# Kernel optimization log

Measured on AMD Instinct MI355X. Metric: run time of the kernel, lower is better.

Reference implementation:

```python
import jax, jax.numpy as jnp
import numpy as np

# Mamba2 derived dims (headdim=64, ngroups=1, mamba_ssm defaults)
D_MODEL = 1024
D_STATE = 64
D_CONV = 4
EXPAND = 2
D_INNER = EXPAND * D_MODEL          # 2048
HEADDIM = 64
NHEADS = D_INNER // HEADDIM          # 32
CONV_DIM = D_INNER + 2 * D_STATE     # 2176 (x, B, C share the depthwise conv)
D_IN_PROJ = 2 * D_INNER + 2 * D_STATE + NHEADS  # 4256 (z, xBC, dt)
BATCH, SEQ = 8, 1024


def setup_inputs() -> dict:
    key = jax.random.key(0)
    ks = jax.random.split(key, 8)
    g = lambda k, shp, sc=0.02: (jax.random.normal(k, shp, jnp.float32) * sc)
    # dt_bias init as in mamba_ssm: inverse-softplus of dt ~ U[1e-3, 1e-1] (log-uniform)
    dt = jnp.exp(jax.random.uniform(ks[3], (NHEADS,), jnp.float32)
                 * (jnp.log(0.1) - jnp.log(0.001)) + jnp.log(0.001))
    dt_bias = dt + jnp.log(-jnp.expm1(-dt))  # softplus^{-1}(dt)
    A_log = jnp.log(jax.random.uniform(ks[4], (NHEADS,), jnp.float32, 1.0, 16.0))
    return {
        "x": jax.random.normal(ks[0], (BATCH, SEQ, D_MODEL), jnp.float32),
        "W_in": g(ks[1], (D_MODEL, D_IN_PROJ)),
        "conv_w": g(ks[2], (D_CONV, CONV_DIM), 0.2),
        "conv_b": jnp.zeros((CONV_DIM,), jnp.float32),
        "dt_bias": dt_bias,
        "A_log": A_log,
        "Dskip": jnp.ones((NHEADS,), jnp.float32),
        "norm_w": jnp.ones((D_INNER,), jnp.float32),
        "W_out": g(ks[5], (D_INNER, D_MODEL)),
        "head_w": g(ks[6], (D_MODEL, 1)),
        "head_b": jnp.zeros((1,), jnp.float32),
    }


def _mamba2(x, W_in, conv_w, conv_b, dt_bias, A_log, Dskip, norm_w, W_out):
    b, l, _ = x.shape
    zxbcdt = x @ W_in                                   # (b, l, 4256)
    z = zxbcdt[..., :D_INNER]
    xBC = zxbcdt[..., D_INNER:D_INNER + CONV_DIM]
    dt = jax.nn.softplus(zxbcdt[..., D_INNER + CONV_DIM:] + dt_bias)  # (b, l, h)
    # causal depthwise conv1d (kernel D_CONV) + SiLU
    pad = jnp.pad(xBC, ((0, 0), (D_CONV - 1, 0), (0, 0)))
    conv = conv_b + sum(pad[:, k:k + l, :] * conv_w[k] for k in range(D_CONV))
    xBC = jax.nn.silu(conv)
    xh = xBC[..., :D_INNER].reshape(b, l, NHEADS, HEADDIM)
    B = xBC[..., D_INNER:D_INNER + D_STATE]             # (b, l, s) ngroups=1
    C = xBC[..., D_INNER + D_STATE:]                    # (b, l, s)
    A = -jnp.exp(A_log)                                 # (h,)
    dA = jnp.exp(dt * A)                                # (b, l, h)

    def step(h, inps):
        dA_t, dt_t, B_t, C_t, x_t = inps                # (b,h),(b,h),(b,s),(b,s),(b,h,p)
        h = h * dA_t[:, :, None, None] + (dt_t[:, :, None] * x_t)[..., None] * B_t[:, None, None, :]
        y = jnp.einsum('bhps,bs->bhp', h, C_t)
        return h, y

    tm = lambda a: jnp.moveaxis(a, 1, 0)                # time-major for scan
    h0 = jnp.zeros((b, NHEADS, HEADDIM, D_STATE), x.dtype)
    _, y = jax.lax.scan(step, h0, (tm(dA), tm(dt), tm(B), tm(C), tm(xh)))
    y = jnp.moveaxis(y, 0, 1) + Dskip[None, None, :, None] * xh   # skip connection
    # gated RMSNorm: norm(y * silu(z)) * weight
    y = y.reshape(b, l, D_INNER) * jax.nn.silu(z)
    y = y * jax.lax.rsqrt(jnp.mean(y * y, axis=-1, keepdims=True) + 1e-5) * norm_w
    return y @ W_out                                    # (b, l, d_model)


def reference(x, W_in, conv_w, conv_b, dt_bias, A_log, Dskip, norm_w, W_out, head_w, head_b):
    y = _mamba2(x, W_in, conv_w, conv_b, dt_bias, A_log, Dskip, norm_w, W_out)
    return y @ head_w + head_b                          # (b, l, 1)
```

## Files before the change

kernel.cpp:

```cpp
#include <hip/hip_runtime.h>
#include <hip/hip_bf16.h>

#define D_MODEL   1024
#define D_STATE   64
#define D_INNER   2048
#define NHEADS    32
#define CONV_DIM  2176
#define D_IN_PROJ 4256
#define NPAD      4352
#define BATCH     8
#define SEQ       1024
#define NROWS     8192
#define NCHUNK    8
#define CLEN      128

typedef __attribute__((ext_vector_type(8))) short bf16x8;
typedef __attribute__((ext_vector_type(4))) float f32x4;

__device__ __forceinline__ float bf2f(unsigned short u){
  unsigned v = ((unsigned)u) << 16;
  return __builtin_bit_cast(float, v);
}
__device__ __forceinline__ unsigned short f2bf(float f){
  __hip_bfloat16 h = __float2bfloat16(f);
  return __builtin_bit_cast(unsigned short, h);
}

__global__ __launch_bounds__(256) void k_prep(const float* __restrict__ x,
                                              const float* __restrict__ W_in,
                                              const float* __restrict__ W_out,
                                              const float* __restrict__ head_w,
                                              const float* __restrict__ norm_w,
                                              unsigned short* __restrict__ xb,
                                              unsigned short* __restrict__ wt,
                                              float* __restrict__ nwc){
  int blk = blockIdx.x;
  if (blk < 8192){
    int i = blk*256 + threadIdx.x;
    float4 v = ((const float4*)x)[i];
    ushort4 o;
    o.x = f2bf(v.x); o.y = f2bf(v.y); o.z = f2bf(v.z); o.w = f2bf(v.w);
    ((ushort4*)xb)[i] = o;
  } else if (blk < 12544){
    __shared__ float tile[32][33];
    int bx = blk - 8192;
    int n0 = (bx % 136) * 32;
    int k0 = (bx / 136) * 32;
    int tx = threadIdx.x & 31;
    int ty = threadIdx.x >> 5;
    #pragma unroll
    for (int i = 0; i < 4; ++i){
      int kk = ty + i*8;
      int n  = n0 + tx;
      tile[kk][tx] = (n < D_IN_PROJ) ? W_in[(size_t)(k0+kk)*D_IN_PROJ + n] : 0.f;
    }
    __syncthreads();
    #pragma unroll
    for (int i = 0; i < 4; ++i){
      int nn = ty + i*8;
      wt[(size_t)(n0+nn)*D_MODEL + k0 + tx] = f2bf(tile[tx][nn]);
    }
  } else {
    int d    = (blk - 12544)*4 + (threadIdx.x >> 6);
    int lane = threadIdx.x & 63;
    const float* row = W_out + (size_t)d * D_MODEL;
    float s = 0.f;
    #pragma unroll
    for (int k = lane; k < D_MODEL; k += 64) s += row[k] * head_w[k];
    #pragma unroll
    for (int off = 32; off; off >>= 1) s += __shfl_down(s, off);
    if (lane == 0) nwc[d] = s * norm_w[d];
  }
}

__global__ __launch_bounds__(512, 1) void k_gemm256(const unsigned short* __restrict__ A,
                                                    const unsigned short* __restrict__ BT,
                                                    unsigned short* __restrict__ C){
  __shared__ unsigned short smem[65536];
  int bid  = blockIdx.x;
  int lt   = (bid & 7) * 68 + (bid >> 3);
  int m0   = (lt / 17) << 8;
  int n0   = (lt % 17) << 8;
  int tid  = threadIdx.x;
  int w    = tid >> 6, lane = tid & 63;
  int wr   = w >> 2, wc = w & 3;
  int stR  = tid >> 3;
  int stCs = (((tid & 7) ^ ((tid >> 3) & 7)) << 3);
  int wb   = w << 9;
  int frow = lane & 15, fk = (lane >> 4) << 3;

  f32x4 acc[8][4];
  #pragma unroll
  for (int i = 0; i < 8; ++i)
    #pragma unroll
    for (int j = 0; j < 4; ++j) acc[i][j] = (f32x4){0.f,0.f,0.f,0.f};

  const unsigned short* sA0 = A  + (size_t)(m0 + stR)*D_MODEL + stCs;
  const unsigned short* sB0 = BT + (size_t)(n0 + stR)*D_MODEL + stCs;

#define GLD(dstOff, src) __builtin_amdgcn_global_load_lds( \
    (const __attribute__((address_space(1))) void*)(src), \
    (__attribute__((address_space(3))) void*)(smem + (dstOff) + wb), 16, 0, 0)
#define ISSA(bb,kt,i) GLD((bb)*32768 + (i)*4096, \
    sA0 + (size_t)(kt)*64 + (size_t)(i)*64*D_MODEL)
#define ISSB(bb,kt,i) GLD((bb)*32768 + 16384 + (i)*4096, \
    sB0 + (size_t)(kt)*64 + (size_t)(i)*64*D_MODEL)
#define RD8(base, r, col) (*(const bf16x8*)((base) + (r)*64 + ((col) ^ (((r)&7)<<3))))

  ISSB(0,0,0); ISSB(0,0,1); ISSB(0,0,2); ISSB(0,0,3);
  ISSA(0,0,0); ISSA(0,0,2); ISSA(0,0,1); ISSA(0,0,3);
  asm volatile("s_waitcnt vmcnt(2)" ::: "memory");
  __builtin_amdgcn_s_barrier();
  asm volatile("" ::: "memory");

  for (int t = 0; t < 16; ++t){
    int cur = t & 1, nxt = cur ^ 1;
    bool iss = (t < 15);
    const unsigned short* At = smem + cur*32768;
    const unsigned short* Bt = At + 16384;

    bf16x8 bF[4][2];
    if (iss){ ISSB(nxt, t+1, 0); ISSB(nxt, t+1, 1); }
    #pragma unroll
    for (int nf = 0; nf < 4; ++nf){
      int r = wc*64 + nf*16 + frow;
      bF[nf][0] = RD8(Bt, r, fk);
      bF[nf][1] = RD8(Bt, r, 32 + fk);
    }
    {
      bf16x8 aF[2][2];
      #pragma unroll
      for (int mi = 0; mi < 2; ++mi){
        int r = wr*128 + mi*16 + frow;
        aF[mi][0] = RD8(At, r, fk);
        aF[mi][1] = RD8(At, r, 32 + fk);
      }
      __builtin_amdgcn_s_setprio(1);
      #pragma unroll
      for (int mi = 0; mi < 2; ++mi)
        #pragma unroll
        for (int nf = 0; nf < 4; ++nf)
          #pragma unroll
          for (int kki = 0; kki < 2; ++kki)
            acc[mi][nf] = __builtin_amdgcn_mfma_f32_16x16x32_bf16(aF[mi][kki], bF[nf][kki], acc[mi][nf], 0, 0, 0);
      __builtin_amdgcn_s_setprio(0);
    }
    if (iss){ ISSB(nxt, t+1, 2); ISSB(nxt, t+1, 3); }
    {
      bf16x8 aF[2][2];
      #pragma unroll
      for (int mi = 0; mi < 2; ++mi){
        int r = wr*128 + (2 + mi)*16 + frow;
        aF[mi][0] = RD8(At, r, fk);
        aF[mi][1] = RD8(At, r, 32 + fk);
      }
      __builtin_amdgcn_s_setprio(1);
      #pragma unroll
      for (int mi = 0; mi < 2; ++mi)
        #pragma unroll
        for (int nf = 0; nf < 4; ++nf)
          #pragma unroll
          for (int kki = 0; kki < 2; ++kki)
            acc[2 + mi][nf] = __builtin_amdgcn_mfma_f32_16x16x32_bf16(aF[mi][kki], bF[nf][kki], acc[2 + mi][nf], 0, 0, 0);
      __builtin_amdgcn_s_setprio(0);
    }
    if (iss) asm volatile("s_waitcnt vmcnt(4)" ::: "memory");
    else     asm volatile("s_waitcnt vmcnt(0)" ::: "memory");
    __builtin_amdgcn_s_barrier();
    asm volatile("" ::: "memory");
    if (iss){ ISSA(nxt, t+1, 0); ISSA(nxt, t+1, 2); }
    {
      bf16x8 aF[2][2];
      #pragma unroll
      for (int mi = 0; mi < 2; ++mi){
        int r = wr*128 + (4 + mi)*16 + frow;
        aF[mi][0] = RD8(At, r, fk);
        aF[mi][1] = RD8(At, r, 32 + fk);
      }
      __builtin_amdgcn_s_setprio(1);
      #pragma unroll
      for (int mi = 0; mi < 2; ++mi)
        #pragma unroll
        for (int nf = 0; nf < 4; ++nf)
          #pragma unroll
          for (int kki = 0; kki < 2; ++kki)
            acc[4 + mi][nf] = __builtin_amdgcn_mfma_f32_16x16x32_bf16(aF[mi][kki], bF[nf][kki], acc[4 + mi][nf], 0, 0, 0);
      __builtin_amdgcn_s_setprio(0);
    }
    if (iss){ ISSA(nxt, t+1, 1); ISSA(nxt, t+1, 3); }
    {
      bf16x8 aF[2][2];
      #pragma unroll
      for (int mi = 0; mi < 2; ++mi){
        int r = wr*128 + (6 + mi)*16 + frow;
        aF[mi][0] = RD8(At, r, fk);
        aF[mi][1] = RD8(At, r, 32 + fk);
      }
      __builtin_amdgcn_s_setprio(1);
      #pragma unroll
      for (int mi = 0; mi < 2; ++mi)
        #pragma unroll
        for (int nf = 0; nf < 4; ++nf)
          #pragma unroll
          for (int kki = 0; kki < 2; ++kki)
            acc[6 + mi][nf] = __builtin_amdgcn_mfma_f32_16x16x32_bf16(aF[mi][kki], bF[nf][kki], acc[6 + mi][nf], 0, 0, 0);
      __builtin_amdgcn_s_setprio(0);
    }
    if (iss) asm volatile("s_waitcnt vmcnt(2)" ::: "memory");
    else     asm volatile("s_waitcnt vmcnt(0)" ::: "memory");
    __builtin_amdgcn_s_barrier();
    asm volatile("" ::: "memory");
  }
#undef GLD
#undef ISSA
#undef ISSB
#undef RD8

  int crow = (lane >> 4) << 2, ccol = lane & 15;
  #pragma unroll
  for (int mf = 0; mf < 8; ++mf)
    #pragma unroll
    for (int nf = 0; nf < 4; ++nf){
      size_t base = (size_t)(m0 + wr*128 + mf*16 + crow)*NPAD + (n0 + wc*64 + nf*16 + ccol);
      #pragma unroll
      for (int r = 0; r < 4; ++r)
        C[base + (size_t)r*NPAD] = f2bf(acc[mf][nf][r]);
    }
}

__global__ __launch_bounds__(64) void k_dtcs(const unsigned short* __restrict__ zx,
                                             const float* __restrict__ dt_bias,
                                             const float* __restrict__ A_log,
                                             float* __restrict__ dtb,
                                             float* __restrict__ csb,
                                             float* __restrict__ cumA){
  int id = blockIdx.x;
  int bh = id >> 3, c = id & 7;
  int b  = bh >> 5, h = bh & 31;
  int l  = threadIdx.x;
  int t0 = c << 7;
  size_t r0 = (size_t)(b*SEQ + t0 + 2*l);
  float bias = dt_bias[h];
  float raw0 = bf2f(zx[r0*NPAD + D_INNER + CONV_DIM + h]) + bias;
  float raw1 = bf2f(zx[(r0+1)*NPAD + D_INNER + CONV_DIM + h]) + bias;
  float d0 = (raw0 > 20.f) ? raw0 : log1pf(expf(raw0));
  float d1 = (raw1 > 20.f) ? raw1 : log1pf(expf(raw1));
  dtb[(size_t)bh*1024 + t0 + 2*l]     = d0;
  dtb[(size_t)bh*1024 + t0 + 2*l + 1] = d1;
  float pr = d0 + d1;
  float s  = pr;
  #pragma unroll
  for (int off = 1; off < 64; off <<= 1){
    float n = __shfl_up(s, off);
    if (l >= off) s += n;
  }
  float excl = s - pr;
  csb[(size_t)id*128 + 2*l]     = excl + d0;
  csb[(size_t)id*128 + 2*l + 1] = excl + pr;
  if (l == 63){
    float A = -expf(A_log[h]);
    cumA[id] = expf(A * s);
  }
}

__global__ __launch_bounds__(256) void k_conv(const unsigned short* __restrict__ zx,
                                              const float* __restrict__ conv_w,
                                              const float* __restrict__ conv_b,
                                              unsigned short* __restrict__ xbc,
                                              unsigned short* __restrict__ bc16){
  int r = blockIdx.x;
  int l = r & (SEQ - 1);
  for (int oc = threadIdx.x; oc < 272; oc += 256){
    int c = oc * 8;
    float acc[8];
    #pragma unroll
    for (int j = 0; j < 8; ++j) acc[j] = conv_b[c + j];
    #pragma unroll
    for (int k = 0; k < 4; ++k){
      int dl = l + k - 3;
      if (dl >= 0){
        bf16x8 v = *(const bf16x8*)(zx + (size_t)(r + k - 3)*NPAD + D_INNER + c);
        #pragma unroll
        for (int j = 0; j < 8; ++j)
          acc[j] = fmaf(bf2f((unsigned short)v[j]), conv_w[k*CONV_DIM + c + j], acc[j]);
      }
    }
    bf16x8 o;
    #pragma unroll
    for (int j = 0; j < 8; ++j){
      float s = acc[j] / (1.f + expf(-acc[j]));
      o[j] = (short)f2bf(s);
    }
    if (c < D_INNER) *(bf16x8*)(xbc  + (size_t)r*D_INNER + c) = o;
    else             *(bf16x8*)(bc16 + (size_t)r*128 + (c - D_INNER)) = o;
  }
}

__global__ __launch_bounds__(256) void k_ssd1(const unsigned short* __restrict__ xbc,
                                              const unsigned short* __restrict__ bc16,
                                              const float* __restrict__ dtb,
                                              const float* __restrict__ csb,
                                              const float* __restrict__ A_log,
                                              unsigned short* __restrict__ hend){
  __shared__ __align__(16) unsigned short XTw[64*136];
  __shared__ __align__(16) unsigned short BTl[64*136];
  int id = blockIdx.x;
  int bh = id >> 3, c = id & 7;
  int b  = bh >> 5, h = bh & 31;
  int tid = threadIdx.x;
  int w = tid >> 6, l = tid & 63;
  float A = -expf(A_log[h]);
  int row0 = b*SEQ + (c << 7);
  float csT = csb[(size_t)id*128 + 127];

  #pragma unroll
  for (int it = 0; it < 4; ++it){
    int idx = it*256 + tid;
    int tau = idx >> 3, pb = idx & 7;
    bf16x8 v = *(const bf16x8*)(xbc + (size_t)(row0+tau)*D_INNER + h*64 + pb*8);
    float wgt = dtb[(size_t)bh*1024 + (c<<7) + tau]
              * expf(A*(csT - csb[(size_t)id*128 + tau]));
    #pragma unroll
    for (int j = 0; j < 8; ++j)
      XTw[(pb*8+j)*136 + tau] = f2bf(bf2f((unsigned short)v[j]) * wgt);
  }
  #pragma unroll
  for (int it = 0; it < 4; ++it){
    int idx = it*256 + tid;
    int tau = idx >> 3, sb = idx & 7;
    bf16x8 v = *(const bf16x8*)(bc16 + (size_t)(row0+tau)*128 + sb*8);
    #pragma unroll
    for (int j = 0; j < 8; ++j)
      BTl[(sb*8+j)*136 + tau] = (unsigned short)v[j];
  }
  __syncthreads();

  int fr = l & 15, fo = (l >> 4) << 3;
  f32x4 acc[4];
  #pragma unroll
  for (int n = 0; n < 4; ++n) acc[n] = (f32x4){0.f,0.f,0.f,0.f};
  #pragma unroll
  for (int kt = 0; kt < 4; ++kt){
    bf16x8 pf = *(const bf16x8*)(XTw + (w*16+fr)*136 + kt*32 + fo);
    #pragma unroll
    for (int n = 0; n < 4; ++n){
      bf16x8 qf = *(const bf16x8*)(BTl + (n*16+fr)*136 + kt*32 + fo);
      acc[n] = __builtin_amdgcn_mfma_f32_16x16x32_bf16(pf, qf, acc[n], 0, 0, 0);
    }
  }
  #pragma unroll
  for (int n = 0; n < 4; ++n)
    #pragma unroll
    for (int r = 0; r < 4; ++r){
      int p = w*16 + ((l>>4)<<2) + r;
      int s = n*16 + fr;
      hend[(size_t)id*4096 + p*64 + s] = f2bf(acc[n][r]);
    }
}

__global__ __launch_bounds__(256) void k_comb(unsigned short* __restrict__ hh,
                                              const float* __restrict__ cumA){
  int bh = blockIdx.x, tid = threadIdx.x;
  float carry[16];
  #pragma unroll
  for (int i = 0; i < 16; ++i) carry[i] = 0.f;
  #pragma unroll
  for (int c = 0; c < NCHUNK; ++c){
    size_t base = (((size_t)bh*NCHUNK + c) << 12) + tid*16;
    bf16x8 a0 = *(const bf16x8*)(hh + base);
    bf16x8 a1 = *(const bf16x8*)(hh + base + 8);
    float ca = cumA[bh*NCHUNK + c];
    float tmp[16];
    #pragma unroll
    for (int i = 0; i < 8; ++i){
      tmp[i]   = bf2f((unsigned short)a0[i]);
      tmp[8+i] = bf2f((unsigned short)a1[i]);
    }
    bf16x8 w0, w1;
    #pragma unroll
    for (int i = 0; i < 8; ++i){
      w0[i] = (short)f2bf(carry[i]);
      w1[i] = (short)f2bf(carry[8+i]);
    }
    *(bf16x8*)(hh + base)     = w0;
    *(bf16x8*)(hh + base + 8) = w1;
    #pragma unroll
    for (int i = 0; i < 16; ++i) carry[i] = tmp[i] + ca*carry[i];
  }
}

__global__ __launch_bounds__(256, 2) void k_ssd2(const unsigned short* __restrict__ xbc,
                                                 const unsigned short* __restrict__ bc16,
                                                 const unsigned short* __restrict__ zx,
                                                 const float* __restrict__ dtb,
                                                 const float* __restrict__ csb,
                                                 const float* __restrict__ A_log,
                                                 const float* __restrict__ Dskip,
                                                 const unsigned short* __restrict__ hbuf,
                                                 unsigned short* __restrict__ yb){
  __shared__ __align__(16) unsigned short Cl[128*72];
  __shared__ __align__(16) unsigned short XTl[64*136];
  __shared__ __align__(16) unsigned short Gm[128*136];
  __shared__ float cs_l[128], dt_l[128], a_l[128];

  int id = blockIdx.x;
  int bh = id >> 3, c = id & 7;
  int b  = bh >> 5, h = bh & 31;
  int tid = threadIdx.x;
  int w = tid >> 6, l = tid & 63;
  float A = -expf(A_log[h]);
  int row0 = b*SEQ + (c << 7);

  #pragma unroll
  for (int it = 0; it < 4; ++it){
    int idx = it*256 + tid;
    int tau = idx >> 3, cb = idx & 7;
    bf16x8 v = *(const bf16x8*)(bc16 + (size_t)(row0+tau)*128 + 64 + cb*8);
    *(bf16x8*)(Cl + tau*72 + cb*8) = v;
  }
  #pragma unroll
  for (int it = 0; it < 4; ++it){
    int idx = it*256 + tid;
    int tau = idx >> 3, pb = idx & 7;
    bf16x8 v = *(const bf16x8*)(xbc + (size_t)(row0+tau)*D_INNER + h*64 + pb*8);
    #pragma unroll
    for (int j = 0; j < 8; ++j)
      XTl[(pb*8+j)*136 + tau] = (unsigned short)v[j];
  }
  if (tid < 128){
    float cs = csb[(size_t)id*128 + tid];
    cs_l[tid] = cs;
    dt_l[tid] = dtb[(size_t)bh*1024 + (c<<7) + tid];
    a_l[tid]  = expf(A*cs);
  }
  __syncthreads();

  int fr = l & 15, fo = (l >> 4) << 3;
  int mtB = 7 - w;

  f32x4 Y[2][4];
  #pragma unroll
  for (int mi = 0; mi < 2; ++mi)
    #pragma unroll
    for (int n = 0; n < 4; ++n) Y[mi][n] = (f32x4){0.f,0.f,0.f,0.f};
  #pragma unroll
  for (int mi = 0; mi < 2; ++mi){
    int mt = mi ? mtB : w;
    #pragma unroll
    for (int kt = 0; kt < 2; ++kt){
      bf16x8 pf = *(const bf16x8*)(Cl + (mt*16+fr)*72 + kt*32 + fo);
      #pragma unroll
      for (int n = 0; n < 4; ++n){
        bf16x8 qf = *(const bf16x8*)(hbuf + (size_t)id*4096 + (n*16+fr)*64 + kt*32 + fo);
        Y[mi][n] = __builtin_amdgcn_mfma_f32_16x16x32_bf16(pf, qf, Y[mi][n], 0, 0, 0);
      }
    }
    #pragma unroll
    for (int r = 0; r < 4; ++r){
      float av = a_l[mt*16 + ((l>>4)<<2) + r];
      #pragma unroll
      for (int n = 0; n < 4; ++n) Y[mi][n][r] *= av;
    }
  }

  f32x4 Sv[9];
  #pragma unroll
  for (int slot = 0; slot < 9; ++slot){
    int mt = (slot <= w) ? w : mtB;
    int nt = (slot <= w) ? slot : slot - w - 1;
    f32x4 acc = (f32x4){0.f,0.f,0.f,0.f};
    #pragma unroll
    for (int kt = 0; kt < 2; ++kt){
      bf16x8 pf = *(const bf16x8*)(Cl + (mt*16+fr)*72 + kt*32 + fo);
      bf16x8 qf = *(const bf16x8*)(bc16 + (size_t)(row0 + nt*16+fr)*128 + kt*32 + fo);
      acc = __builtin_amdgcn_mfma_f32_16x16x32_bf16(pf, qf, acc, 0, 0, 0);
    }
    int tau = nt*16 + fr;
    float dtt = dt_l[tau];
    float cst = cs_l[tau];
    #pragma unroll
    for (int r = 0; r < 4; ++r){
      int t = mt*16 + ((l>>4)<<2) + r;
      float v = acc[r] * dtt * expf(A*(cs_l[t] - cst));
      acc[r] = (tau <= t) ? v : 0.f;
    }
    Sv[slot] = acc;
  }

  #pragma unroll
  for (int slot = 0; slot < 9; ++slot){
    int mt = (slot <= w) ? w : mtB;
    int nt = (slot <= w) ? slot : slot - w - 1;
    int tau = nt*16 + fr;
    #pragma unroll
    for (int r = 0; r < 4; ++r){
      int t = mt*16 + ((l>>4)<<2) + r;
      Gm[t*136 + tau] = f2bf(Sv[slot][r]);
    }
  }
  {
    int mtE = (w & 1) ? mtB : w;
    int ntE = mtE + 1;
    #pragma unroll
    for (int r = 0; r < 4; ++r){
      int t = mtE*16 + ((l>>4)<<2) + r;
      Gm[t*136 + ntE*16 + fr] = 0;
    }
  }
  __syncthreads();

  #pragma unroll
  for (int mi = 0; mi < 2; ++mi){
    int mt = mi ? mtB : w;
    int kmax = (mt + 2) >> 1;
    for (int kt2 = 0; kt2 < kmax; ++kt2){
      bf16x8 pf = *(const bf16x8*)(Gm + (mt*16+fr)*136 + kt2*32 + fo);
      #pragma unroll
      for (int n = 0; n < 4; ++n){
        bf16x8 qf = *(const bf16x8*)(XTl + (n*16+fr)*136 + kt2*32 + fo);
        Y[mi][n] = __builtin_amdgcn_mfma_f32_16x16x32_bf16(pf, qf, Y[mi][n], 0, 0, 0);
      }
    }
  }

  float dsk = Dskip[h];
  #pragma unroll
  for (int mi = 0; mi < 2; ++mi){
    int mt = mi ? mtB : w;
    #pragma unroll
    for (int r = 0; r < 4; ++r){
      int t = mt*16 + ((l>>4)<<2) + r;
      size_t orow = (size_t)(row0 + t)*D_INNER + h*64;
      size_t zrow = (size_t)(row0 + t)*NPAD + h*64;
      #pragma unroll
      for (int n = 0; n < 4; ++n){
        int p = n*16 + fr;
        float xv = bf2f(XTl[p*136 + t]);
        float zf = bf2f(zx[zrow + p]);
        float yv = Y[mi][n][r] + dsk*xv;
        float g  = yv * (zf / (1.f + expf(-zf)));
        yb[orow + p] = f2bf(g);
      }
    }
  }
}

__global__ __launch_bounds__(256) void k_epilogue(const unsigned short* __restrict__ yg,
                                                  const float* __restrict__ nwc,
                                                  const float* __restrict__ head_b,
                                                  float* __restrict__ out){
  int r   = blockIdx.x;
  int tid = threadIdx.x;
  bf16x8 y8 = *(const bf16x8*)(yg + (size_t)r*D_INNER + tid*8);
  float4 w0 = ((const float4*)nwc)[tid*2];
  float4 w1 = ((const float4*)nwc)[tid*2 + 1];
  float wv[8] = {w0.x, w0.y, w0.z, w0.w, w1.x, w1.y, w1.z, w1.w};
  float s2 = 0.f, sd = 0.f;
  #pragma unroll
  for (int k = 0; k < 8; ++k){
    float g = bf2f((unsigned short)y8[k]);
    s2 += g*g; sd += g*wv[k];
  }
  #pragma unroll
  for (int off = 32; off; off >>= 1){
    s2 += __shfl_down(s2, off);
    sd += __shfl_down(sd, off);
  }
  __shared__ float r2[4], rd[4];
  if ((tid & 63) == 0){ r2[tid >> 6] = s2; rd[tid >> 6] = sd; }
  __syncthreads();
  if (tid == 0){
    float t2 = r2[0] + r2[1] + r2[2] + r2[3];
    float td = rd[0] + rd[1] + rd[2] + rd[3];
    out[r] = rsqrtf(t2 * (1.f/2048.f) + 1e-5f) * td + head_b[0];
  }
}

extern "C" void kernel_launch(void* const* d_in, const int* in_sizes, int n_in,
                              void* d_out, int out_size, void* d_ws, size_t ws_size,
                              hipStream_t stream){
  const float* x       = (const float*)d_in[0];
  const float* W_in    = (const float*)d_in[1];
  const float* conv_w  = (const float*)d_in[2];
  const float* conv_b  = (const float*)d_in[3];
  const float* dt_bias = (const float*)d_in[4];
  const float* A_log   = (const float*)d_in[5];
  const float* Dskip   = (const float*)d_in[6];
  const float* norm_w  = (const float*)d_in[7];
  const float* W_out   = (const float*)d_in[8];
  const float* head_w  = (const float*)d_in[9];
  const float* head_b  = (const float*)d_in[10];
  float* out = (float*)d_out;

  char* ws = (char*)d_ws;
  unsigned short* xb   = (unsigned short*)(ws + 0);
  unsigned short* wt   = (unsigned short*)(ws + 16777216);
  unsigned short* zx16 = (unsigned short*)(ws + 25690112);
  unsigned short* xbc  = (unsigned short*)(ws + 96993280);
  float*          dtb  = (float*)         (ws + 132644864);
  float*          nwc  = (float*)         (ws + 134742016);
  unsigned short* yb   = (unsigned short*)(ws + 134750208);

  unsigned short* hbuf = xb;
  unsigned short* bc16 = wt;
  float*          csb  = (float*)(ws + 16777216 + 2097152);
  float*          cumA = (float*)(ws + 16777216 + 3145728);

  k_prep<<<13056, 256, 0, stream>>>(x, W_in, W_out, head_w, norm_w, xb, wt, nwc);
  k_gemm256<<<(NROWS/256)*(NPAD/256), 512, 0, stream>>>(xb, wt, zx16);
  k_dtcs<<<2048, 64, 0, stream>>>(zx16, dt_bias, A_log, dtb, csb, cumA);
  k_conv<<<NROWS, 256, 0, stream>>>(zx16, conv_w, conv_b, xbc, bc16);
  k_ssd1<<<2048, 256, 0, stream>>>(xbc, bc16, dtb, csb, A_log, hbuf);
  k_comb<<<256, 256, 0, stream>>>(hbuf, cumA);
  k_ssd2<<<2048, 256, 0, stream>>>(xbc, bc16, zx16, dtb, csb, A_log, Dskip, hbuf, yb);
  k_epilogue<<<NROWS, 256, 0, stream>>>(yb, nwc, head_b, out);
}
```

Baseline: 242.0 us.

## Fuse RMSNorm and head reductions into SSD output stage via atomics

The SSD output kernel now computes per-row partial sums of g^2 and g·(norm_w·W_out·head_w) directly. It reduces them across lanes and accumulates them into a small global buffer with atomicAdd, so the bf16 gated-y tensor is no longer written and re-read by a separate epilogue kernel. A tiny k_out kernel finishes the rsqrt and head bias, and k_dtcs zeroes the accumulator buffer. The conv kernel's block-to-row mapping is also permuted to interleave batches. The atomics add contention and make the floating-point summation order nondeterministic.

```diff
diff --git a/kernel.cpp b/kernel.cpp
--- a/kernel.cpp
+++ b/kernel.cpp
@@ -233,11 +233,14 @@
                                              const float* __restrict__ A_log,
                                              float* __restrict__ dtb,
                                              float* __restrict__ csb,
-                                             float* __restrict__ cumA){
+                                             float* __restrict__ cumA,
+                                             float* __restrict__ s2sd){
   int id = blockIdx.x;
   int bh = id >> 3, c = id & 7;
   int b  = bh >> 5, h = bh & 31;
   int l  = threadIdx.x;
+  int gid = id*64 + l;
+  if (gid < 16384) s2sd[gid] = 0.f;
   int t0 = c << 7;
   size_t r0 = (size_t)(b*SEQ + t0 + 2*l);
   float bias = dt_bias[h];
@@ -268,7 +271,8 @@
                                               const float* __restrict__ conv_b,
                                               unsigned short* __restrict__ xbc,
                                               unsigned short* __restrict__ bc16){
-  int r = blockIdx.x;
+  int bid = blockIdx.x;
+  int r = ((bid & 7) << 10) | (bid >> 3);
   int l = r & (SEQ - 1);
   for (int oc = threadIdx.x; oc < 272; oc += 256){
     int c = oc * 8;
@@ -396,8 +400,9 @@
                                                  const float* __restrict__ csb,
                                                  const float* __restrict__ A_log,
                                                  const float* __restrict__ Dskip,
+                                                 const float* __restrict__ nwc,
                                                  const unsigned short* __restrict__ hbuf,
-                                                 unsigned short* __restrict__ yb){
+                                                 float* __restrict__ s2sd){
   __shared__ __align__(16) unsigned short Cl[128*72];
   __shared__ __align__(16) unsigned short XTl[64*136];
   __shared__ __align__(16) unsigned short Gm[128*136];
@@ -524,14 +529,19 @@
   }
 
   float dsk = Dskip[h];
+  float nw[4];
+  #pragma unroll
+  for (int n = 0; n < 4; ++n) nw[n] = nwc[h*64 + n*16 + fr];
+  float* s2b = s2sd;
+  float* sdb = s2sd + NROWS;
   #pragma unroll
   for (int mi = 0; mi < 2; ++mi){
     int mt = mi ? mtB : w;
     #pragma unroll
     for (int r = 0; r < 4; ++r){
       int t = mt*16 + ((l>>4)<<2) + r;
-      size_t orow = (size_t)(row0 + t)*D_INNER + h*64;
       size_t zrow = (size_t)(row0 + t)*NPAD + h*64;
+      float s2p = 0.f, sdp = 0.f;
       #pragma unroll
       for (int n = 0; n < 4; ++n){
         int p = n*16 + fr;
@@ -539,41 +549,28 @@
         float zf = bf2f(zx[zrow + p]);
         float yv = Y[mi][n][r] + dsk*xv;
         float g  = yv * (zf / (1.f + expf(-zf)));
-        yb[orow + p] = f2bf(g);
-      }
-    }
-  }
-}
-
-__global__ __launch_bounds__(256) void k_epilogue(const unsigned short* __restrict__ yg,
-                                                  const float* __restrict__ nwc,
-                                                  const float* __restrict__ head_b,
-                                                  float* __restrict__ out){
-  int r   = blockIdx.x;
-  int tid = threadIdx.x;
-  bf16x8 y8 = *(const bf16x8*)(yg + (size_t)r*D_INNER + tid*8);
-  float4 w0 = ((const float4*)nwc)[tid*2];
-  float4 w1 = ((const float4*)nwc)[tid*2 + 1];
-  float wv[8] = {w0.x, w0.y, w0.z, w0.w, w1.x, w1.y, w1.z, w1.w};
-  float s2 = 0.f, sd = 0.f;
-  #pragma unroll
-  for (int k = 0; k < 8; ++k){
-    float g = bf2f((unsigned short)y8[k]);
-    s2 += g*g; sd += g*wv[k];
-  }
-  #pragma unroll
-  for (int off = 32; off; off >>= 1){
-    s2 += __shfl_down(s2, off);
-    sd += __shfl_down(sd, off);
-  }
-  __shared__ float r2[4], rd[4];
-  if ((tid & 63) == 0){ r2[tid >> 6] = s2; rd[tid >> 6] = sd; }
-  __syncthreads();
-  if (tid == 0){
-    float t2 = r2[0] + r2[1] + r2[2] + r2[3];
-    float td = rd[0] + rd[1] + rd[2] + rd[3];
-    out[r] = rsqrtf(t2 * (1.f/2048.f) + 1e-5f) * td + head_b[0];
-  }
+        s2p += g*g; sdp += g*nw[n];
+      }
+      #pragma unroll
+      for (int off = 1; off < 16; off <<= 1){
+        s2p += __shfl_xor(s2p, off);
+        sdp += __shfl_xor(sdp, off);
+      }
+      if (fr == 0){
+        atomicAdd(&s2b[row0 + t], s2p);
+        atomicAdd(&sdb[row0 + t], sdp);
+      }
+    }
+  }
+}
+
+__global__ __launch_bounds__(256) void k_out(const float* __restrict__ s2sd,
+                                             const float* __restrict__ head_b,
+                                             float* __restrict__ out){
+  int r = blockIdx.x*256 + threadIdx.x;
+  float s2 = s2sd[r];
+  float sd = s2sd[NROWS + r];
+  out[r] = rsqrtf(s2 * (1.f/2048.f) + 1e-5f) * sd + head_b[0];
 }
 
 extern "C" void kernel_launch(void* const* d_in, const int* in_sizes, int n_in,
@@ -599,7 +596,7 @@
   unsigned short* xbc  = (unsigned short*)(ws + 96993280);
   float*          dtb  = (float*)         (ws + 132644864);
   float*          nwc  = (float*)         (ws + 134742016);
-  unsigned short* yb   = (unsigned short*)(ws + 134750208);
+  float*          s2sd = (float*)         (ws + 134750208);
 
   unsigned short* hbuf = xb;
   unsigned short* bc16 = wt;
@@ -608,10 +605,10 @@
 
   k_prep<<<13056, 256, 0, stream>>>(x, W_in, W_out, head_w, norm_w, xb, wt, nwc);
   k_gemm256<<<(NROWS/256)*(NPAD/256), 512, 0, stream>>>(xb, wt, zx16);
-  k_dtcs<<<2048, 64, 0, stream>>>(zx16, dt_bias, A_log, dtb, csb, cumA);
+  k_dtcs<<<2048, 64, 0, stream>>>(zx16, dt_bias, A_log, dtb, csb, cumA, s2sd);
   k_conv<<<NROWS, 256, 0, stream>>>(zx16, conv_w, conv_b, xbc, bc16);
   k_ssd1<<<2048, 256, 0, stream>>>(xbc, bc16, dtb, csb, A_log, hbuf);
   k_comb<<<256, 256, 0, stream>>>(hbuf, cumA);
-  k_ssd2<<<2048, 256, 0, stream>>>(xbc, bc16, zx16, dtb, csb, A_log, Dskip, hbuf, yb);
-  k_epilogue<<<NROWS, 256, 0, stream>>>(yb, nwc, head_b, out);
-}
+  k_ssd2<<<2048, 256, 0, stream>>>(xbc, bc16, zx16, dtb, csb, A_log, Dskip, nwc, hbuf, s2sd);
+  k_out<<<NROWS/256, 256, 0, stream>>>(s2sd, head_b, out);
+}
```

New measurement: 244.5 us. No clear change (+1.0%).
